# Optimization experiments

Hardware: AMD Instinct MI355X
Metric: run time of the kernel (lower is better)

## Reference

```python
import jax, jax.numpy as jnp
import numpy as np


def setup_inputs() -> dict:
    key = jax.random.key(0)
    ks = jax.random.split(key, 8)
    B, A = 2048, 64
    STATE, ACT = 5, 4
    d_in = STATE + ACT  # 9
    x = jax.random.normal(ks[0], (B, STATE), dtype=jnp.float32)
    actions = jax.random.normal(ks[1], (A, ACT), dtype=jnp.float32)
    def lin(k, fin, fout):
        return jax.random.normal(k, (fin, fout), dtype=jnp.float32) / np.sqrt(fin)
    W1 = lin(ks[2], d_in, 128); b1 = jnp.zeros((128,), jnp.float32)
    W2 = lin(ks[3], 128, 1024); b2 = jnp.zeros((1024,), jnp.float32)
    W3 = lin(ks[4], 1024, 1024); b3 = jnp.zeros((1024,), jnp.float32)
    W4 = lin(ks[5], 1024, 128); b4 = jnp.zeros((128,), jnp.float32)
    W5 = lin(ks[6], 128, 1); b5 = jnp.zeros((1,), jnp.float32)
    return {"x": x, "actions": actions,
            "W1": W1, "b1": b1, "W2": W2, "b2": b2, "W3": W3, "b3": b3,
            "W4": W4, "b4": b4, "W5": W5, "b5": b5}


def reference(x, actions, W1, b1, W2, b2, W3, b3, W4, b4, W5, b5):
    # x: [B,5] states; actions: [A,4] candidate actions.
    # Equivalent to the original's per-sample per-action loop: evaluate the
    # 5-layer Tanh MLP on concat(state, action) for every (sample, action) pair.
    B = x.shape[0]
    A = actions.shape[0]
    s = jnp.broadcast_to(x[:, None, :], (B, A, x.shape[1]))
    a = jnp.broadcast_to(actions[None, :, :], (B, A, actions.shape[1]))
    inp = jnp.concatenate([s, a], axis=-1)  # [B,A,9]
    h = jnp.tanh(inp @ W1 + b1)
    h = jnp.tanh(h @ W2 + b2)
    h = jnp.tanh(h @ W3 + b3)
    h = jnp.tanh(h @ W4 + b4)
    values = (h @ W5 + b5)[..., 0]  # [B,A]
    best = jnp.argmax(values, axis=1)  # [B]
    max_value_action = actions[best]  # [B,4]
    return (max_value_action, values)
```

## Files before the change

kernel.cpp:

```cpp
#include <hip/hip_runtime.h>
#include <hip/hip_bf16.h>
#include <math.h>


typedef short bf16x8 __attribute__((ext_vector_type(8)));
typedef float f32x4 __attribute__((ext_vector_type(4)));
typedef float f32x16 __attribute__((ext_vector_type(16)));

__device__ __host__ inline unsigned short f2bf(float f) {
    union { float f; unsigned u; } v; v.f = f;
    unsigned r = v.u + 0x7fff + ((v.u >> 16) & 1);
    return (unsigned short)(r >> 16);
}
__device__ inline unsigned short cvt_bf16(float f) {
    __hip_bfloat16 h = __float2bfloat16(f);
    return *reinterpret_cast<unsigned short*>(&h);
}
__device__ inline float bf2f(unsigned short b) {
    union { unsigned u; float f; } v; v.u = ((unsigned)b) << 16;
    return v.f;
}
__device__ inline float fast_tanh(float x) {
    float e = __expf(2.0f * x);
    return 1.0f - 2.0f * __builtin_amdgcn_rcpf(e + 1.0f);
}

#define DELTA 0.025f
#define ITEM_CAP 16384

struct WLE { unsigned s, base, nc, pad; };

#define HSWZ(row, b) ((b) ^ (((row) & 15) << 4))

__global__ __launch_bounds__(256) void pack_all(
    const float* __restrict__ W2, const float* __restrict__ W3, const float* __restrict__ W4,
    unsigned short* __restrict__ W2p, unsigned short* __restrict__ W3p,
    unsigned short* __restrict__ W4p, unsigned* __restrict__ cnts)
{
    int tid = blockIdx.x * 256 + threadIdx.x;
    if (tid < 2) cnts[tid] = 0u;
    int blob = tid >> 6, lane = tid & 63;
    if (blob >= 2560) return;
    bf16x8 v;
    if (blob < 256) {
        int nt = blob >> 2, kt = blob & 3;
        int n = nt * 16 + (lane & 15);
        int kbase = kt * 32 + ((lane >> 4) & 3) * 8;
        #pragma unroll
        for (int e = 0; e < 8; ++e) v[e] = (short)f2bf(W2[(size_t)(kbase + e) * 1024 + n]);
        *(bf16x8*)&W2p[(size_t)blob * 512 + lane * 8] = v;
    } else if (blob < 2304) {
        int lb = blob - 256;
        int nt = lb >> 6, kt = lb & 63;
        int n = nt * 32 + (lane & 31);
        int kbase = kt * 16 + (lane >> 5) * 8;
        #pragma unroll
        for (int e = 0; e < 8; ++e) v[e] = (short)f2bf(W3[(size_t)(kbase + e) * 1024 + n]);
        *(bf16x8*)&W3p[(size_t)lb * 512 + lane * 8] = v;
    } else {
        int lb = blob - 2304;
        int nt = lb >> 5, kt = lb & 31;
        int n = nt * 16 + (lane & 15);
        int kbase = kt * 32 + ((lane >> 4) & 3) * 8;
        #pragma unroll
        for (int e = 0; e < 8; ++e) v[e] = (short)f2bf(W4[(size_t)(kbase + e) * 128 + n]);
        *(bf16x8*)&W4p[(size_t)lb * 512 + lane * 8] = v;
    }
}

__global__ __launch_bounds__(1024, 4) void qnet_mfma(
    const float* __restrict__ x, const float* __restrict__ actions,
    const float* __restrict__ W1, const float* __restrict__ b1,
    const float* __restrict__ b2, const float* __restrict__ b3,
    const float* __restrict__ b4,
    const float* __restrict__ W5, const float* __restrict__ b5,
    const unsigned short* __restrict__ W2p,
    const unsigned short* __restrict__ W3p,
    const unsigned short* __restrict__ W4p,
    float* __restrict__ values, float* __restrict__ out_actions,
    unsigned* __restrict__ cnts, WLE* __restrict__ wl,
    unsigned* __restrict__ items)
{
    __shared__ unsigned short h2[64 * 1024];
    __shared__ unsigned short hc[64 * 128];

    const int t = threadIdx.x;
    const int lane = t & 63;
    const int wave = t >> 6;
    const int p0 = blockIdx.x * 64;
    const int kb16 = (lane >> 4) * 16;
    const int kb32 = (lane >> 5) * 16;

    {
        int r = t >> 4;
        int c0 = (t & 15) * 8;
        const float* xs = &x[blockIdx.x * 5];
        const float* as = &actions[r * 4];
        float in[9] = { xs[0], xs[1], xs[2], xs[3], xs[4], as[0], as[1], as[2], as[3] };
        #pragma unroll
        for (int j = 0; j < 8; ++j) {
            int c = c0 + j;
            float acc = b1[c];
            #pragma unroll
            for (int k = 0; k < 9; ++k) acc += in[k] * W1[k * 128 + c];
            *(unsigned short*)((char*)hc + r * 256 + HSWZ(r, c * 2)) = cvt_bf16(fast_tanh(acc));
        }
    }
    __syncthreads();

    {
        bf16x8 Af[4][4];
        #pragma unroll
        for (int rt = 0; rt < 4; ++rt)
            #pragma unroll
            for (int ks = 0; ks < 4; ++ks) {
                int row = rt * 16 + (lane & 15);
                Af[rt][ks] = *(const bf16x8*)((const char*)hc + row * 256 + HSWZ(row, ks * 64 + kb16));
            }
        #pragma unroll
        for (int j = 0; j < 4; ++j) {
            int nT = wave * 4 + j;
            float bv = b2[nT * 16 + (lane & 15)];
            f32x4 acc0 = (f32x4){ bv, bv, bv, bv };
            f32x4 acc1 = acc0, acc2 = acc0, acc3v = acc0;
            #pragma unroll
            for (int ks = 0; ks < 4; ++ks) {
                bf16x8 b = *(const bf16x8*)&W2p[((size_t)(nT * 4 + ks)) * 512 + lane * 8];
                acc0 = __builtin_amdgcn_mfma_f32_16x16x32_bf16(Af[0][ks], b, acc0, 0, 0, 0);
                acc1 = __builtin_amdgcn_mfma_f32_16x16x32_bf16(Af[1][ks], b, acc1, 0, 0, 0);
                acc2 = __builtin_amdgcn_mfma_f32_16x16x32_bf16(Af[2][ks], b, acc2, 0, 0, 0);
                acc3v = __builtin_amdgcn_mfma_f32_16x16x32_bf16(Af[3][ks], b, acc3v, 0, 0, 0);
            }
            int n = nT * 16 + (lane & 15);
            #pragma unroll
            for (int rr = 0; rr < 4; ++rr) {
                int m0 = (lane >> 4) * 4 + rr;
                *(unsigned short*)((char*)h2 + (m0 +  0) * 2048 + HSWZ(m0 +  0, n * 2)) = cvt_bf16(fast_tanh(acc0[rr]));
                *(unsigned short*)((char*)h2 + (m0 + 16) * 2048 + HSWZ(m0 + 16, n * 2)) = cvt_bf16(fast_tanh(acc1[rr]));
                *(unsigned short*)((char*)h2 + (m0 + 32) * 2048 + HSWZ(m0 + 32, n * 2)) = cvt_bf16(fast_tanh(acc2[rr]));
                *(unsigned short*)((char*)h2 + (m0 + 48) * 2048 + HSWZ(m0 + 48, n * 2)) = cvt_bf16(fast_tanh(acc3v[rr]));
            }
        }
    }
    __syncthreads();

    f32x16 a00, a01, a10, a11;
    {
        float bv0 = b3[wave * 64 + (lane & 31)];
        float bv1 = b3[wave * 64 + 32 + (lane & 31)];
        #pragma unroll
        for (int i = 0; i < 16; ++i) { a00[i] = bv0; a10[i] = bv0; a01[i] = bv1; a11[i] = bv1; }
    }
    const int r0 = lane & 31, r1 = 32 + (lane & 31);
    {
        const unsigned short* bbase = &W3p[((size_t)(wave * 2) * 64) * 512 + lane * 8];
        #pragma unroll 2
        for (int kt = 0; kt < 64; ++kt) {
            bf16x8 A0 = *(const bf16x8*)((const char*)h2 + r0 * 2048 + HSWZ(r0, kt * 32 + kb32));
            bf16x8 A1 = *(const bf16x8*)((const char*)h2 + r1 * 2048 + HSWZ(r1, kt * 32 + kb32));
            bf16x8 B0 = *(const bf16x8*)(bbase + (size_t)kt * 512);
            bf16x8 B1 = *(const bf16x8*)(bbase + (size_t)(64 + kt) * 512);
            a00 = __builtin_amdgcn_mfma_f32_32x32x16_bf16(A0, B0, a00, 0, 0, 0);
            a10 = __builtin_amdgcn_mfma_f32_32x32x16_bf16(A1, B0, a10, 0, 0, 0);
            a01 = __builtin_amdgcn_mfma_f32_32x32x16_bf16(A0, B1, a01, 0, 0, 0);
            a11 = __builtin_amdgcn_mfma_f32_32x32x16_bf16(A1, B1, a11, 0, 0, 0);
        }
    }
    __syncthreads();

    {
        int c0l = wave * 64 + (lane & 31);
        #pragma unroll
        for (int r = 0; r < 16; ++r) {
            int row = (r & 3) + 8 * (r >> 2) + 4 * (lane >> 5);
            int rowB = row + 32;
            *(unsigned short*)((char*)h2 + row  * 2048 + HSWZ(row,  c0l * 2)) = cvt_bf16(fast_tanh(a00[r]));
            *(unsigned short*)((char*)h2 + rowB * 2048 + HSWZ(rowB, c0l * 2)) = cvt_bf16(fast_tanh(a10[r]));
            *(unsigned short*)((char*)h2 + row  * 2048 + HSWZ(row,  (c0l + 32) * 2)) = cvt_bf16(fast_tanh(a01[r]));
            *(unsigned short*)((char*)h2 + rowB * 2048 + HSWZ(rowB, (c0l + 32) * 2)) = cvt_bf16(fast_tanh(a11[r]));
        }
    }
    __syncthreads();

    {
        const int ct = wave & 7, rtp = wave >> 3;
        const int rowA = rtp * 32 + (lane & 15);
        const int rowB = rowA + 16;
        float bv = b4[ct * 16 + (lane & 15)];
        f32x4 acc4a = (f32x4){ bv, bv, bv, bv };
        f32x4 acc4b = acc4a;
        #pragma unroll 4
        for (int k32 = 0; k32 < 32; ++k32) {
            bf16x8 B = *(const bf16x8*)&W4p[((size_t)(ct * 32 + k32)) * 512 + lane * 8];
            bf16x8 aA = *(const bf16x8*)((const char*)h2 + rowA * 2048 + HSWZ(rowA, k32 * 64 + kb16));
            bf16x8 aB = *(const bf16x8*)((const char*)h2 + rowB * 2048 + HSWZ(rowB, k32 * 64 + kb16));
            acc4a = __builtin_amdgcn_mfma_f32_16x16x32_bf16(aA, B, acc4a, 0, 0, 0);
            acc4b = __builtin_amdgcn_mfma_f32_16x16x32_bf16(aB, B, acc4b, 0, 0, 0);
        }
        int n = ct * 16 + (lane & 15);
        #pragma unroll
        for (int rr = 0; rr < 4; ++rr) {
            int mA = rtp * 32 + (lane >> 4) * 4 + rr;
            int mB = mA + 16;
            *(unsigned short*)((char*)hc + mA * 256 + HSWZ(mA, n * 2)) = cvt_bf16(fast_tanh(acc4a[rr]));
            *(unsigned short*)((char*)hc + mB * 256 + HSWZ(mB, n * 2)) = cvt_bf16(fast_tanh(acc4b[rr]));
        }
    }
    __syncthreads();

    float* vbuf = (float*)&h2[0];
    {
        int r = t >> 4, g = t & 15;
        float part = 0.0f;
        #pragma unroll
        for (int j = 0; j < 8; ++j) {
            int cidx = g * 8 + j;
            unsigned short hb = *(const unsigned short*)((const char*)hc + r * 256 + HSWZ(r, cidx * 2));
            part += bf2f(hb) * W5[cidx];
        }
        part += __shfl_down(part, 8);
        part += __shfl_down(part, 4);
        part += __shfl_down(part, 2);
        part += __shfl_down(part, 1);
        if (g == 0) {
            float val = part + b5[0];
            values[p0 + r] = val;
            vbuf[r] = val;
        }
    }
    __syncthreads();

    if (t < 64) {
        float myv = vbuf[t];
        float v = myv; int idx = t;
        #pragma unroll
        for (int off = 32; off; off >>= 1) {
            float ov = __shfl_down(v, off);
            int oi = __shfl_down(idx, off);
            if (ov > v || (ov == v && oi < idx)) { v = ov; idx = oi; }
        }
        float vm = __shfl(v, 0);
        int best = __shfl(idx, 0);
        if (t < 4) out_actions[blockIdx.x * 4 + t] = actions[best * 4 + t];
        unsigned long long mask = __ballot(myv >= vm - DELTA);
        int nc = __popcll(mask);
        if (nc > 1) {
            unsigned base = 0;
            if (t == 0) base = atomicAdd(&cnts[1], (unsigned)nc);
            base = (unsigned)__shfl((int)base, 0);
            if (base + (unsigned)nc <= (unsigned)ITEM_CAP) {
                if (t == 0) {
                    unsigned slot = atomicAdd(&cnts[0], 1u);
                    wl[slot].s = blockIdx.x; wl[slot].base = base; wl[slot].nc = (unsigned)nc;
                }
                if (myv >= vm - DELTA) {
                    int rank = __popcll(mask & ((1ull << t) - 1ull));
                    items[base + rank] = ((unsigned)blockIdx.x << 6) | (unsigned)t;
                }
            }
        }
    }
}

__global__ __launch_bounds__(256) void fixup_eval(
    const float* __restrict__ x, const float* __restrict__ actions,
    const float* __restrict__ W1, const float* __restrict__ b1,
    const float* __restrict__ W2, const float* __restrict__ b2,
    const float* __restrict__ W3, const float* __restrict__ b3,
    const float* __restrict__ W4, const float* __restrict__ b4,
    const float* __restrict__ W5, const float* __restrict__ b5,
    const unsigned* __restrict__ cnts, const unsigned* __restrict__ items,
    float* __restrict__ vexact)
{
    __shared__ float h1s[8][128];
    __shared__ float h2s[8][1024];
    __shared__ float h3s[8][1024];
    __shared__ float h4s[8][128];
    __shared__ float xin[8][5];
    __shared__ float ain[8][4];

    const int t = threadIdx.x;
    int n = (int)cnts[1]; if (n > ITEM_CAP) n = ITEM_CAP;
    int nb = (n + 7) >> 3;
    for (int b = blockIdx.x; b < nb; b += gridDim.x) {
        if (t < 8) {
            int idx = b * 8 + t;
            unsigned it = items[(idx < n) ? idx : (b * 8)];
            int s = (int)((it >> 6) & 2047), a = (int)(it & 63);
            #pragma unroll
            for (int k = 0; k < 5; ++k) xin[t][k] = x[s * 5 + k];
            #pragma unroll
            for (int k = 0; k < 4; ++k) ain[t][k] = actions[a * 4 + k];
        }
        __syncthreads();
        {
            int r = t >> 5, cb = (t & 31) * 4;
            #pragma unroll
            for (int j = 0; j < 4; ++j) {
                int c = cb + j;
                float acc = b1[c];
                #pragma unroll
                for (int k = 0; k < 5; ++k) acc += xin[r][k] * W1[k * 128 + c];
                #pragma unroll
                for (int k = 0; k < 4; ++k) acc += ain[r][k] * W1[(5 + k) * 128 + c];
                h1s[r][c] = tanhf(acc);
            }
        }
        __syncthreads();
        {
            int cb = t * 4;
            float acc[8][4];
            float4 bv = *(const float4*)&b2[cb];
            #pragma unroll
            for (int r = 0; r < 8; ++r) { acc[r][0]=bv.x; acc[r][1]=bv.y; acc[r][2]=bv.z; acc[r][3]=bv.w; }
            for (int k = 0; k < 128; ++k) {
                float4 w = *(const float4*)&W2[k * 1024 + cb];
                #pragma unroll
                for (int r = 0; r < 8; ++r) {
                    float hv = h1s[r][k];
                    acc[r][0] += hv * w.x; acc[r][1] += hv * w.y;
                    acc[r][2] += hv * w.z; acc[r][3] += hv * w.w;
                }
            }
            #pragma unroll
            for (int r = 0; r < 8; ++r) {
                h2s[r][cb+0] = tanhf(acc[r][0]); h2s[r][cb+1] = tanhf(acc[r][1]);
                h2s[r][cb+2] = tanhf(acc[r][2]); h2s[r][cb+3] = tanhf(acc[r][3]);
            }
        }
        __syncthreads();
        {
            int cb = t * 4;
            float acc[8][4];
            float4 bv = *(const float4*)&b3[cb];
            #pragma unroll
            for (int r = 0; r < 8; ++r) { acc[r][0]=bv.x; acc[r][1]=bv.y; acc[r][2]=bv.z; acc[r][3]=bv.w; }
            for (int k = 0; k < 1024; ++k) {
                float4 w = *(const float4*)&W3[k * 1024 + cb];
                #pragma unroll
                for (int r = 0; r < 8; ++r) {
                    float hv = h2s[r][k];
                    acc[r][0] += hv * w.x; acc[r][1] += hv * w.y;
                    acc[r][2] += hv * w.z; acc[r][3] += hv * w.w;
                }
            }
            #pragma unroll
            for (int r = 0; r < 8; ++r) {
                h3s[r][cb+0] = tanhf(acc[r][0]); h3s[r][cb+1] = tanhf(acc[r][1]);
                h3s[r][cb+2] = tanhf(acc[r][2]); h3s[r][cb+3] = tanhf(acc[r][3]);
            }
        }
        __syncthreads();
        {
            int r = t >> 5, cb = (t & 31) * 4;
            float acc[4];
            float4 bv = *(const float4*)&b4[cb];
            acc[0]=bv.x; acc[1]=bv.y; acc[2]=bv.z; acc[3]=bv.w;
            for (int k = 0; k < 1024; ++k) {
                float4 w = *(const float4*)&W4[k * 128 + cb];
                float hv = h3s[r][k];
                acc[0] += hv * w.x; acc[1] += hv * w.y; acc[2] += hv * w.z; acc[3] += hv * w.w;
            }
            h4s[r][cb+0] = tanhf(acc[0]); h4s[r][cb+1] = tanhf(acc[1]);
            h4s[r][cb+2] = tanhf(acc[2]); h4s[r][cb+3] = tanhf(acc[3]);
        }
        __syncthreads();
        if (t < 8) {
            float acc = b5[0];
            for (int k = 0; k < 128; ++k) acc += h4s[t][k] * W5[k];
            int idx = b * 8 + t;
            if (idx < n) vexact[idx] = acc;
        }
        __syncthreads();
    }
}

__global__ __launch_bounds__(256) void finalize_argmax(
    const unsigned* __restrict__ cnts, const WLE* __restrict__ wl,
    const unsigned* __restrict__ items, const float* __restrict__ vexact,
    const float* __restrict__ actions, float* __restrict__ out_actions)
{
    int gw = (blockIdx.x * 256 + threadIdx.x) >> 6;
    int lane = threadIdx.x & 63;
    int nwl = (int)cnts[0]; if (nwl > 2048) nwl = 2048;
    if (gw >= nwl) return;
    unsigned s = wl[gw].s, base = wl[gw].base, nc = wl[gw].nc;
    float v = (lane < (int)nc) ? vexact[base + lane] : -3.0e38f;
    int idx = lane;
    #pragma unroll
    for (int off = 32; off; off >>= 1) {
        float ov = __shfl_down(v, off);
        int oi = __shfl_down(idx, off);
        if (ov > v || (ov == v && oi < idx)) { v = ov; idx = oi; }
    }
    int i0 = __shfl(idx, 0);
    int a = (int)(items[base + i0] & 63);
    if (lane < 4) out_actions[s * 4 + lane] = actions[a * 4 + lane];
}

#define TR 16
__global__ __launch_bounds__(256) void qnet_fused(
    const float* __restrict__ x, const float* __restrict__ actions,
    const float* __restrict__ W1, const float* __restrict__ b1,
    const float* __restrict__ W2, const float* __restrict__ b2,
    const float* __restrict__ W3, const float* __restrict__ b3,
    const float* __restrict__ W4, const float* __restrict__ b4,
    const float* __restrict__ W5, const float* __restrict__ b5,
    float* __restrict__ values)
{
    __shared__ float h_small[TR][128];
    __shared__ float hA[TR][1024];
    __shared__ float hB[TR][1024];
    const int t = threadIdx.x;
    const int p0 = blockIdx.x * TR;
    for (int i = t; i < TR * 128; i += 256) {
        int r = i >> 7, c = i & 127;
        int p = p0 + r;
        int bidx = p >> 6, aidx = p & 63;
        float acc = b1[c];
        for (int k = 0; k < 5; ++k) acc += x[bidx * 5 + k] * W1[k * 128 + c];
        for (int k = 0; k < 4; ++k) acc += actions[aidx * 4 + k] * W1[(5 + k) * 128 + c];
        h_small[r][c] = tanhf(acc);
    }
    __syncthreads();
    {
        const int c0 = t * 4;
        float4 bias = *(const float4*)&b2[c0];
        float acc[TR][4];
        for (int r = 0; r < TR; ++r) { acc[r][0]=bias.x; acc[r][1]=bias.y; acc[r][2]=bias.z; acc[r][3]=bias.w; }
        for (int k = 0; k < 128; k += 4) {
            float4 w0 = *(const float4*)&W2[(k+0)*1024+c0];
            float4 w1 = *(const float4*)&W2[(k+1)*1024+c0];
            float4 w2 = *(const float4*)&W2[(k+2)*1024+c0];
            float4 w3 = *(const float4*)&W2[(k+3)*1024+c0];
            for (int r = 0; r < TR; ++r) {
                float4 hv = *(const float4*)&h_small[r][k];
                acc[r][0] += hv.x*w0.x + hv.y*w1.x + hv.z*w2.x + hv.w*w3.x;
                acc[r][1] += hv.x*w0.y + hv.y*w1.y + hv.z*w2.y + hv.w*w3.y;
                acc[r][2] += hv.x*w0.z + hv.y*w1.z + hv.z*w2.z + hv.w*w3.z;
                acc[r][3] += hv.x*w0.w + hv.y*w1.w + hv.z*w2.w + hv.w*w3.w;
            }
        }
        for (int r = 0; r < TR; ++r) {
            hA[r][c0+0]=tanhf(acc[r][0]); hA[r][c0+1]=tanhf(acc[r][1]);
            hA[r][c0+2]=tanhf(acc[r][2]); hA[r][c0+3]=tanhf(acc[r][3]);
        }
    }
    __syncthreads();
    {
        const int c0 = t * 4;
        float4 bias = *(const float4*)&b3[c0];
        float acc[TR][4];
        for (int r = 0; r < TR; ++r) { acc[r][0]=bias.x; acc[r][1]=bias.y; acc[r][2]=bias.z; acc[r][3]=bias.w; }
        for (int k = 0; k < 1024; k += 4) {
            float4 w0 = *(const float4*)&W3[(k+0)*1024+c0];
            float4 w1 = *(const float4*)&W3[(k+1)*1024+c0];
            float4 w2 = *(const float4*)&W3[(k+2)*1024+c0];
            float4 w3 = *(const float4*)&W3[(k+3)*1024+c0];
            for (int r = 0; r < TR; ++r) {
                float4 hv = *(const float4*)&hA[r][k];
                acc[r][0] += hv.x*w0.x + hv.y*w1.x + hv.z*w2.x + hv.w*w3.x;
                acc[r][1] += hv.x*w0.y + hv.y*w1.y + hv.z*w2.y + hv.w*w3.y;
                acc[r][2] += hv.x*w0.z + hv.y*w1.z + hv.z*w2.z + hv.w*w3.z;
                acc[r][3] += hv.x*w0.w + hv.y*w1.w + hv.z*w2.w + hv.w*w3.w;
            }
        }
        for (int r = 0; r < TR; ++r) {
            hB[r][c0+0]=tanhf(acc[r][0]); hB[r][c0+1]=tanhf(acc[r][1]);
            hB[r][c0+2]=tanhf(acc[r][2]); hB[r][c0+3]=tanhf(acc[r][3]);
        }
    }
    __syncthreads();
    {
        const int c = t & 127;
        const int rh = t >> 7;
        float acc[8];
        float bias = b4[c];
        for (int r = 0; r < 8; ++r) acc[r] = bias;
        for (int k = 0; k < 1024; k += 4) {
            float w0 = W4[(k+0)*128+c], w1 = W4[(k+1)*128+c];
            float w2 = W4[(k+2)*128+c], w3 = W4[(k+3)*128+c];
            for (int r = 0; r < 8; ++r) {
                float4 hv = *(const float4*)&hB[rh*8+r][k];
                acc[r] += hv.x*w0 + hv.y*w1 + hv.z*w2 + hv.w*w3;
            }
        }
        for (int r = 0; r < 8; ++r) h_small[rh*8+r][c] = tanhf(acc[r]);
    }
    __syncthreads();
    if (t < TR) {
        float acc = b5[0];
        for (int k = 0; k < 128; k += 4) {
            float4 hv = *(const float4*)&h_small[t][k];
            float4 wv = *(const float4*)&W5[k];
            acc += hv.x*wv.x + hv.y*wv.y + hv.z*wv.z + hv.w*wv.w;
        }
        values[p0 + t] = acc;
    }
}

__global__ __launch_bounds__(256) void argmax_gather(
    const float* __restrict__ values, const float* __restrict__ actions,
    float* __restrict__ out_actions)
{
    const int wave = threadIdx.x >> 6;
    const int lane = threadIdx.x & 63;
    const int state = blockIdx.x * (blockDim.x >> 6) + wave;
    float v = values[state * 64 + lane];
    int idx = lane;
    for (int off = 32; off; off >>= 1) {
        float ov = __shfl_down(v, off);
        int oi = __shfl_down(idx, off);
        if (ov > v || (ov == v && oi < idx)) { v = ov; idx = oi; }
    }
    idx = __shfl(idx, 0);
    if (lane < 4) out_actions[state * 4 + lane] = actions[idx * 4 + lane];
}

extern "C" void kernel_launch(void* const* d_in, const int* in_sizes, int n_in,
                              void* d_out, int out_size, void* d_ws, size_t ws_size,
                              hipStream_t stream) {
    const float* x       = (const float*)d_in[0];
    const float* actions = (const float*)d_in[1];
    const float* W1 = (const float*)d_in[2];  const float* b1 = (const float*)d_in[3];
    const float* W2 = (const float*)d_in[4];  const float* b2 = (const float*)d_in[5];
    const float* W3 = (const float*)d_in[6];  const float* b3 = (const float*)d_in[7];
    const float* W4 = (const float*)d_in[8];  const float* b4 = (const float*)d_in[9];
    const float* W5 = (const float*)d_in[10]; const float* b5 = (const float*)d_in[11];

    float* out_actions = (float*)d_out;
    float* values      = (float*)d_out + 2048 * 4;

    const size_t nW2 = 128 * 1024, nW3 = 1024 * 1024, nW4 = 1024 * 128;
    const size_t wbytes = (nW2 + nW3 + nW4) * sizeof(unsigned short);
    const size_t need = wbytes + 16 + 2048 * sizeof(WLE) + ITEM_CAP * 4 + ITEM_CAP * 4;

    if (ws_size >= need) {
        unsigned short* W2p = (unsigned short*)d_ws;
        unsigned short* W3p = W2p + nW2;
        unsigned short* W4p = W3p + nW3;
        char* p = (char*)d_ws + wbytes;
        unsigned* cnts = (unsigned*)p;                 p += 16;
        WLE* wl = (WLE*)p;                             p += 2048 * sizeof(WLE);
        unsigned* items = (unsigned*)p;                p += ITEM_CAP * 4;
        float* vexact = (float*)p;

        pack_all<<<640, 256, 0, stream>>>(W2, W3, W4, W2p, W3p, W4p, cnts);
        qnet_mfma<<<2048, 1024, 0, stream>>>(x, actions, W1, b1, b2, b3, b4, W5, b5,
                                             W2p, W3p, W4p, values, out_actions,
                                             cnts, wl, items);
        fixup_eval<<<512, 256, 0, stream>>>(x, actions, W1, b1, W2, b2, W3, b3,
                                            W4, b4, W5, b5, cnts, items, vexact);
        finalize_argmax<<<512, 256, 0, stream>>>(cnts, wl, items, vexact,
                                                 actions, out_actions);
    } else {
        qnet_fused<<<2048 * 64 / TR, 256, 0, stream>>>(x, actions, W1, b1, W2, b2, W3, b3,
                                                       W4, b4, W5, b5, values);
        argmax_gather<<<2048 / 4, 256, 0, stream>>>(values, actions, out_actions);
    }
}
```

Measured before the change: 594.5 us.

## Batch 16 fixup items per block and stream layer 3 into layer 4 by chunks

The exact-precision fixup kernel now runs 512 threads and evaluates 16 candidate items per block instead of 8. This halves how often the fp32 W2/W3/W4 weights are reread per item. Layer 3 is computed in two 512-column chunks, and each chunk is consumed right away by layer 4, so the full h3 buffer is no longer kept in shared memory. The final dot product uses a wave shuffle reduction instead of 8 serial threads. In exchange, each thread keeps more accumulators live, there are extra barriers, and fewer blocks are busy when the candidate list is small.

```diff
diff --git a/kernel.cpp b/kernel.cpp
--- a/kernel.cpp
+++ b/kernel.cpp
@@ -262,7 +262,7 @@
     }
 }
 
-__global__ __launch_bounds__(256) void fixup_eval(
+__global__ __launch_bounds__(512) void fixup_eval(
     const float* __restrict__ x, const float* __restrict__ actions,
     const float* __restrict__ W1, const float* __restrict__ b1,
     const float* __restrict__ W2, const float* __restrict__ b2,
@@ -272,20 +272,20 @@
     const unsigned* __restrict__ cnts, const unsigned* __restrict__ items,
     float* __restrict__ vexact)
 {
-    __shared__ float h1s[8][128];
-    __shared__ float h2s[8][1024];
-    __shared__ float h3s[8][1024];
-    __shared__ float h4s[8][128];
-    __shared__ float xin[8][5];
-    __shared__ float ain[8][4];
+    __shared__ float h1s[16][128];
+    __shared__ float h2s[16][1024];
+    __shared__ float h3c[16][512];
+    __shared__ float h4s[16][128];
+    __shared__ float xin[16][5];
+    __shared__ float ain[16][4];
 
     const int t = threadIdx.x;
     int n = (int)cnts[1]; if (n > ITEM_CAP) n = ITEM_CAP;
-    int nb = (n + 7) >> 3;
+    int nb = (n + 15) >> 4;
     for (int b = blockIdx.x; b < nb; b += gridDim.x) {
-        if (t < 8) {
-            int idx = b * 8 + t;
-            unsigned it = items[(idx < n) ? idx : (b * 8)];
+        if (t < 16) {
+            int idx = b * 16 + t;
+            unsigned it = items[(idx < n) ? idx : (b * 16)];
             int s = (int)((it >> 6) & 2047), a = (int)(it & 63);
             #pragma unroll
             for (int k = 0; k < 5; ++k) xin[t][k] = x[s * 5 + k];
@@ -308,68 +308,79 @@
         }
         __syncthreads();
         {
-            int cb = t * 4;
-            float acc[8][4];
-            float4 bv = *(const float4*)&b2[cb];
-            #pragma unroll
-            for (int r = 0; r < 8; ++r) { acc[r][0]=bv.x; acc[r][1]=bv.y; acc[r][2]=bv.z; acc[r][3]=bv.w; }
+            int c0 = t * 2;
+            float2 acc[16];
+            float2 bv = *(const float2*)&b2[c0];
+            #pragma unroll
+            for (int r = 0; r < 16; ++r) acc[r] = bv;
             for (int k = 0; k < 128; ++k) {
-                float4 w = *(const float4*)&W2[k * 1024 + cb];
+                float2 w = *(const float2*)&W2[k * 1024 + c0];
                 #pragma unroll
-                for (int r = 0; r < 8; ++r) {
+                for (int r = 0; r < 16; ++r) {
                     float hv = h1s[r][k];
-                    acc[r][0] += hv * w.x; acc[r][1] += hv * w.y;
-                    acc[r][2] += hv * w.z; acc[r][3] += hv * w.w;
+                    acc[r].x += hv * w.x; acc[r].y += hv * w.y;
                 }
             }
             #pragma unroll
-            for (int r = 0; r < 8; ++r) {
-                h2s[r][cb+0] = tanhf(acc[r][0]); h2s[r][cb+1] = tanhf(acc[r][1]);
-                h2s[r][cb+2] = tanhf(acc[r][2]); h2s[r][cb+3] = tanhf(acc[r][3]);
-            }
+            for (int r = 0; r < 16; ++r) {
+                h2s[r][c0] = tanhf(acc[r].x);
+                h2s[r][c0 + 1] = tanhf(acc[r].y);
+            }
+        }
+        __syncthreads();
+        float acc4[4];
+        {
+            float bv4 = b4[t & 127];
+            #pragma unroll
+            for (int rr = 0; rr < 4; ++rr) acc4[rr] = bv4;
+        }
+        #pragma unroll 1
+        for (int ch = 0; ch < 2; ++ch) {
+            {
+                int c = ch * 512 + t;
+                float acc[16];
+                float bv = b3[c];
+                #pragma unroll
+                for (int r = 0; r < 16; ++r) acc[r] = bv;
+                for (int k = 0; k < 1024; ++k) {
+                    float w = W3[k * 1024 + c];
+                    #pragma unroll
+                    for (int r = 0; r < 16; ++r) acc[r] += h2s[r][k] * w;
+                }
+                #pragma unroll
+                for (int r = 0; r < 16; ++r) h3c[r][t] = tanhf(acc[r]);
+            }
+            __syncthreads();
+            {
+                int c4 = t & 127, rb = (t >> 7) * 4;
+                for (int k = 0; k < 512; ++k) {
+                    float w = W4[(ch * 512 + k) * 128 + c4];
+                    #pragma unroll
+                    for (int rr = 0; rr < 4; ++rr) acc4[rr] += h3c[rb + rr][k] * w;
+                }
+            }
+            __syncthreads();
+        }
+        {
+            int c4 = t & 127, rb = (t >> 7) * 4;
+            #pragma unroll
+            for (int rr = 0; rr < 4; ++rr) h4s[rb + rr][c4] = tanhf(acc4[rr]);
         }
         __syncthreads();
         {
-            int cb = t * 4;
-            float acc[8][4];
-            float4 bv = *(const float4*)&b3[cb];
-            #pragma unroll
-            for (int r = 0; r < 8; ++r) { acc[r][0]=bv.x; acc[r][1]=bv.y; acc[r][2]=bv.z; acc[r][3]=bv.w; }
-            for (int k = 0; k < 1024; ++k) {
-                float4 w = *(const float4*)&W3[k * 1024 + cb];
-                #pragma unroll
-                for (int r = 0; r < 8; ++r) {
-                    float hv = h2s[r][k];
-                    acc[r][0] += hv * w.x; acc[r][1] += hv * w.y;
-                    acc[r][2] += hv * w.z; acc[r][3] += hv * w.w;
-                }
-            }
-            #pragma unroll
-            for (int r = 0; r < 8; ++r) {
-                h3s[r][cb+0] = tanhf(acc[r][0]); h3s[r][cb+1] = tanhf(acc[r][1]);
-                h3s[r][cb+2] = tanhf(acc[r][2]); h3s[r][cb+3] = tanhf(acc[r][3]);
-            }
-        }
-        __syncthreads();
-        {
-            int r = t >> 5, cb = (t & 31) * 4;
-            float acc[4];
-            float4 bv = *(const float4*)&b4[cb];
-            acc[0]=bv.x; acc[1]=bv.y; acc[2]=bv.z; acc[3]=bv.w;
-            for (int k = 0; k < 1024; ++k) {
-                float4 w = *(const float4*)&W4[k * 128 + cb];
-                float hv = h3s[r][k];
-                acc[0] += hv * w.x; acc[1] += hv * w.y; acc[2] += hv * w.z; acc[3] += hv * w.w;
-            }
-            h4s[r][cb+0] = tanhf(acc[0]); h4s[r][cb+1] = tanhf(acc[1]);
-            h4s[r][cb+2] = tanhf(acc[2]); h4s[r][cb+3] = tanhf(acc[3]);
-        }
-        __syncthreads();
-        if (t < 8) {
-            float acc = b5[0];
-            for (int k = 0; k < 128; ++k) acc += h4s[t][k] * W5[k];
-            int idx = b * 8 + t;
-            if (idx < n) vexact[idx] = acc;
+            int r = t >> 5, g = t & 31;
+            float part = 0.0f;
+            #pragma unroll
+            for (int j = 0; j < 4; ++j) part += h4s[r][g * 4 + j] * W5[g * 4 + j];
+            part += __shfl_down(part, 16);
+            part += __shfl_down(part, 8);
+            part += __shfl_down(part, 4);
+            part += __shfl_down(part, 2);
+            part += __shfl_down(part, 1);
+            if (g == 0) {
+                int idx = b * 16 + r;
+                if (idx < n) vexact[idx] = part + b5[0];
+            }
         }
         __syncthreads();
     }
@@ -549,7 +560,7 @@
         qnet_mfma<<<2048, 1024, 0, stream>>>(x, actions, W1, b1, b2, b3, b4, W5, b5,
                                              W2p, W3p, W4p, values, out_actions,
                                              cnts, wl, items);
-        fixup_eval<<<512, 256, 0, stream>>>(x, actions, W1, b1, W2, b2, W3, b3,
+        fixup_eval<<<512, 512, 0, stream>>>(x, actions, W1, b1, W2, b2, W3, b3,
                                             W4, b4, W5, b5, cnts, items, vexact);
         finalize_argmax<<<512, 256, 0, stream>>>(cnts, wl, items, vexact,
                                                  actions, out_actions);
```

After: 690.6 us. +16.2%, slower.
